# Optimization experiments

Measured on AMD Instinct MI355X. Metric: run time of the kernel, lower is better.

## Reference

```python
import jax, jax.numpy as jnp
import numpy as np

DIM = 256
NUM_ITERS = 5
NUM_CLASSES = 365
TRIU_LEN = DIM * (DIM + 1) // 2  # 32896

# lower-triangular (incl. diag) flat indices in row-major order, matching
# torch.ones(d,d).triu().t().reshape(-1).nonzero()
_TRIL_IDX = np.nonzero(np.tril(np.ones((DIM, DIM), np.bool_)).reshape(-1))[0]


def setup_inputs() -> dict:
    key = jax.random.key(0)
    k1, k2 = jax.random.split(key)
    B = 64
    x = jax.random.normal(k1, (B, DIM, 14, 14), dtype=jnp.float32)
    fc_w = jax.random.normal(k2, (NUM_CLASSES, TRIU_LEN), dtype=jnp.float32) * 0.01
    fc_b = jnp.zeros((NUM_CLASSES,), dtype=jnp.float32)
    return {"x": x, "fc_w": fc_w, "fc_b": fc_b}


def _cov(x):
    # x: [B, D, H, W] -> centered second-order pooling [B, D, D]
    B, D, H, W = x.shape
    M = H * W
    xf = x.reshape(B, D, M)
    xc = xf - jnp.mean(xf, axis=2, keepdims=True)
    # x @ I_hat @ x^T == (xc @ xf^T) / M == (xc @ xc^T) / M
    y = jnp.einsum('bdm,bem->bde', xc, xc) / M
    return y + 1e-7 * jnp.eye(D, dtype=x.dtype)


def _matrix_sqrt_ns(a, num_iters):
    # Newton-Schulz iteration for matrix square root; a: [B, D, D]
    B, D, _ = a.shape
    I = jnp.eye(D, dtype=a.dtype)
    normA = jnp.trace(a, axis1=1, axis2=2)  # [B]
    Y = a / normA[:, None, None]
    Z = jnp.broadcast_to(I, (B, D, D))
    for _ in range(num_iters):
        T = 0.5 * (3.0 * I - jnp.einsum('bij,bjk->bik', Z, Y))
        Y = jnp.einsum('bij,bjk->bik', Y, T)
        Z = jnp.einsum('bij,bjk->bik', T, Z)
    return Y * jnp.sqrt(normA)[:, None, None]


def _triu(x):
    # gather lower-tri (== upper-tri of symmetric cov) entries: [B, D, D] -> [B, D(D+1)/2]
    B, D, _ = x.shape
    return x.reshape(B, D * D)[:, _TRIL_IDX]


def reference(x, fc_w, fc_b):
    y = _cov(x)
    y = _matrix_sqrt_ns(y, NUM_ITERS)
    y = _triu(y)
    return y @ fc_w.T + fc_b
```

## Files before the change

### kernel.cpp

```cpp
#include <hip/hip_runtime.h>
#include <hip/hip_bf16.h>

typedef __attribute__((ext_vector_type(8))) short bf16x8;
typedef __attribute__((ext_vector_type(4))) float f32x4;

static __device__ __forceinline__ ushort f2b(float f) {
    unsigned u = __float_as_uint(f);
    return (ushort)((u + 0x7fffu + ((u >> 16) & 1u)) >> 16);
}

static __device__ __forceinline__ void gload16(const void* g, void* lds) {
    __builtin_amdgcn_global_load_lds(
        (const __attribute__((address_space(1))) unsigned int*)g,
        (__attribute__((address_space(3))) unsigned int*)lds, 16, 0, 0);
}

__global__ __launch_bounds__(256) void prep_kernel(
    const float* __restrict__ x, ushort* __restrict__ xc, float* __restrict__ var)
{
    const int t = threadIdx.x, wv = t >> 6, l = t & 63;
    const int bid = blockIdx.x;
    const int x8 = bid & 7, rr = bid >> 3;
    const int dgrp = rr & 63, bgrp = rr >> 6;
    const int b = bgrp * 8 + x8;
    const int rowid = b * 256 + dgrp * 4 + wv;
    const float* xr = x + (size_t)rowid * 196;

    float x0 = xr[l];
    float x1 = xr[l + 64];
    float x2 = xr[l + 128];
    float x3 = (l < 4) ? xr[l + 192] : 0.0f;

    float s1 = x0 + x1 + x2 + x3;
    float s2 = x0*x0 + x1*x1 + x2*x2 + x3*x3;
    #pragma unroll
    for (int off = 32; off; off >>= 1) {
        s1 += __shfl_xor(s1, off);
        s2 += __shfl_xor(s2, off);
    }
    const float mean = s1 * (1.0f / 196.0f);
    if (l == 0) var[rowid] = s2 * (1.0f / 196.0f) - mean * mean + 1e-7f;

    ushort* xcr = xc + (size_t)rowid * 256;
    xcr[l]       = f2b(x0 - mean);
    xcr[l + 64]  = f2b(x1 - mean);
    xcr[l + 128] = f2b(x2 - mean);
    xcr[l + 192] = (l < 4) ? f2b(x3 - mean) : (ushort)0;
}

template<int MODE>
__global__ __launch_bounds__(256) void gemm_ns(
    const ushort* __restrict__ A, const ushort* __restrict__ A2,
    const ushort* __restrict__ Bt,
    ushort* __restrict__ C, ushort* __restrict__ C2,
    const float* __restrict__ var)
{
    __shared__ ushort As[2][2][128][32];
    __shared__ ushort Bs[2][2][128][32];
    __shared__ float tr_s[4];

    const int bid = blockIdx.x, x8 = bid & 7;
    int b, i0, j0;
    bool useA2 = false;
    if (MODE == 2) {
        const int tt = (bid >> 3) & 3;
        useA2 = ((bid >> 5) & 1) != 0;
        b = (bid >> 6) * 8 + x8;
        i0 = (tt >> 1) * 128; j0 = (tt & 1) * 128;
    } else if (MODE == 3) {
        const int rr = bid >> 3, t3 = rr % 3;
        b = (rr / 3) * 8 + x8;
        i0 = (t3 == 0) ? 0 : 128;
        j0 = (t3 == 2) ? 128 : 0;
    } else {
        const int tt = (bid >> 3) & 3;
        b = (bid >> 5) * 8 + x8;
        i0 = (tt >> 1) * 128; j0 = (tt & 1) * 128;
    }
    const ushort* Ab  = (useA2 ? A2 : A) + (size_t)b * 65536;
    const ushort* Btb = Bt + (size_t)b * 65536;

    const int t = threadIdx.x, wv = t >> 6, l = t & 63;
    const int li = l & 15, hi = l >> 4;
    const int wr = wv >> 1, wc = wv & 1;
    const int lrow = l >> 2;
    const int seg = (l & 3) * 8;

#define STAGE(buf, ck) do {                                                     \
    _Pragma("unroll")                                                           \
    for (int it = 0; it < 4; ++it) {                                            \
        const int c16 = wv * 4 + it;                                 \
        const int tk = c16 >> 3, r16 = c16 & 7;                                 \
        const int row = r16 * 16 + lrow;                                        \
        gload16(Ab + (size_t)(i0 + row) * 256 + (ck) * 64 + tk * 32 + seg,      \
                (char*)&As[buf][0][0][0] + tk * 8192 + r16 * 1024);             \
        gload16(Btb + (size_t)(j0 + row) * 256 + (ck) * 64 + tk * 32 + seg,     \
                (char*)&Bs[buf][0][0][0] + tk * 8192 + r16 * 1024);             \
    }                                                                           \
} while (0)

    STAGE(0, 0);
    if (MODE == 0 || MODE == 3) {
        float v = var[b * 256 + t];
        #pragma unroll
        for (int off = 32; off; off >>= 1) v += __shfl_xor(v, off);
        if (l == 0) tr_s[wv] = v;
    }
    __syncthreads();
    float trace = 0.f;
    if (MODE == 0 || MODE == 3) trace = tr_s[0] + tr_s[1] + tr_s[2] + tr_s[3];

    f32x4 acc[4][4];
    #pragma unroll
    for (int m = 0; m < 4; ++m)
        #pragma unroll
        for (int n = 0; n < 4; ++n) acc[m][n] = (f32x4){0.f, 0.f, 0.f, 0.f};

    int cur = 0;
    #pragma unroll
    for (int ck = 0; ck < 4; ++ck) {
        if (ck < 3) STAGE(cur ^ 1, ck + 1);
        #pragma unroll
        for (int s = 0; s < 2; ++s) {
            bf16x8 af[4], bfr[4];
            #pragma unroll
            for (int m = 0; m < 4; ++m)
                af[m] = *(const bf16x8*)&As[cur][s][wr * 64 + m * 16 + li][hi * 8];
            #pragma unroll
            for (int n = 0; n < 4; ++n)
                bfr[n] = *(const bf16x8*)&Bs[cur][s][wc * 64 + n * 16 + li][hi * 8];
            #pragma unroll
            for (int m = 0; m < 4; ++m)
                #pragma unroll
                for (int n = 0; n < 4; ++n)
                    acc[m][n] = __builtin_amdgcn_mfma_f32_16x16x32_bf16(
                        af[m], bfr[n], acc[m][n], 0, 0, 0);
        }
        __syncthreads();
        cur ^= 1;
    }
#undef STAGE

    if (MODE == 3) {
        const float sc = sqrtf(trace);
        ushort* trib = C + (size_t)b * 32896;
        #pragma unroll
        for (int m = 0; m < 4; ++m)
            #pragma unroll
            for (int n = 0; n < 4; ++n)
                #pragma unroll
                for (int r = 0; r < 4; ++r) {
                    const int gi = i0 + wr * 64 + m * 16 + hi * 4 + r;
                    const int gj = j0 + wc * 64 + n * 16 + li;
                    if (gj <= gi)
                        trib[(gi * (gi + 1)) / 2 + gj] = f2b(acc[m][n][r] * sc);
                }
    } else {
        const float invtr = (MODE == 0) ? (1.0f / trace) : 0.0f;
        ushort* Cb  = ((MODE == 2 && useA2) ? C2 : C) + (size_t)b * 65536;
        ushort* C2b = (MODE == 0) ? (C2 + (size_t)b * 65536) : nullptr;
        #pragma unroll
        for (int m = 0; m < 4; ++m)
            #pragma unroll
            for (int n = 0; n < 4; ++n)
                #pragma unroll
                for (int r = 0; r < 4; ++r) {
                    const int gi = i0 + wr * 64 + m * 16 + hi * 4 + r;
                    const int gj = j0 + wc * 64 + n * 16 + li;
                    const float v = acc[m][n][r];
                    const size_t idx = (size_t)gi * 256 + gj;
                    if (MODE == 0) {
                        float y0 = (v * (1.0f / 196.0f) + ((gi == gj) ? 1e-7f : 0.0f)) * invtr;
                        Cb[idx]  = f2b(y0);
                        C2b[idx] = f2b(((gi == gj) ? 1.5f : 0.0f) - 0.5f * y0);
                    } else if (MODE == 1) {
                        Cb[idx] = f2b(((gi == gj) ? 1.5f : 0.0f) - 0.5f * v);
                    } else {
                        Cb[idx] = f2b(v);
                    }
                }
    }
}

__global__ __launch_bounds__(256) void fc_gemm(
    const ushort* __restrict__ tri, const float* __restrict__ W,
    float* __restrict__ partial)
{
    __shared__ ushort Asl[4][64][32];
    __shared__ float  Wsl[4][64][32];

    const int ntile = blockIdx.x;
    const int split = blockIdx.y;
    const int steps = 12 + (split < 8 ? 1 : 0);
    const int step0 = split * 12 + (split < 8 ? split : 8);

    const int tid = threadIdx.x, wv = tid >> 6, l = tid & 63;
    const int li = l & 15, hi = l >> 4;

    const int arow = tid >> 2, aseg = tid & 3;
    const int wrow0 = tid >> 3, wseg = tid & 7;
    const int wrow1 = 32 + (tid >> 3);
    const int wcl0 = min(ntile * 64 + wrow0, 364);
    const int wcl1 = min(ntile * 64 + wrow1, 364);

#define FSTAGE(s) do {                                                          \
    const int kk_ = (step0 + (s)) * 32;                                         \
    const int r_ = (s) & 3;                                                     \
    gload16(tri + (size_t)arow * 32896 + kk_ + aseg * 8,                        \
            &Asl[r_][arow][aseg * 8]);                                          \
    gload16(W + (size_t)wcl0 * 32896 + kk_ + wseg * 4,                          \
            &Wsl[r_][wrow0][wseg * 4]);                                         \
    gload16(W + (size_t)wcl1 * 32896 + kk_ + wseg * 4,                          \
            &Wsl[r_][wrow1][wseg * 4]);                                         \
} while (0)

    FSTAGE(0); FSTAGE(1); FSTAGE(2);

    f32x4 acc[4];
    #pragma unroll
    for (int m = 0; m < 4; ++m) acc[m] = (f32x4){0.f, 0.f, 0.f, 0.f};

    for (int s = 0; s < steps; ++s) {
        if (s + 3 < steps) FSTAGE(s + 3);
        asm volatile("s_waitcnt vmcnt(9)" ::: "memory");
        __builtin_amdgcn_sched_barrier(0);
        __builtin_amdgcn_s_barrier();

        const int r = s & 3;
        const float4 wf0 = *(const float4*)&Wsl[r][wv * 16 + li][hi * 8];
        const float4 wf1 = *(const float4*)&Wsl[r][wv * 16 + li][hi * 8 + 4];
        bf16x8 bfr;
        bfr[0] = (short)f2b(wf0.x); bfr[1] = (short)f2b(wf0.y);
        bfr[2] = (short)f2b(wf0.z); bfr[3] = (short)f2b(wf0.w);
        bfr[4] = (short)f2b(wf1.x); bfr[5] = (short)f2b(wf1.y);
        bfr[6] = (short)f2b(wf1.z); bfr[7] = (short)f2b(wf1.w);

        bf16x8 af[4];
        #pragma unroll
        for (int m = 0; m < 4; ++m)
            af[m] = *(const bf16x8*)&Asl[r][m * 16 + li][hi * 8];
        #pragma unroll
        for (int m = 0; m < 4; ++m)
            acc[m] = __builtin_amdgcn_mfma_f32_16x16x32_bf16(af[m], bfr, acc[m], 0, 0, 0);

        __builtin_amdgcn_s_barrier();
    }
#undef FSTAGE

    #pragma unroll
    for (int m = 0; m < 4; ++m)
        #pragma unroll
        for (int rr = 0; rr < 4; ++rr) {
            const int i = m * 16 + hi * 4 + rr;
            const int j = ntile * 64 + wv * 16 + li;
            partial[((size_t)split * 64 + i) * 384 + j] = acc[m][rr];
        }
}

__global__ void fc_reduce(const float* __restrict__ partial,
                          const float* __restrict__ bias, float* __restrict__ out)
{
    const int idx = blockIdx.x * 256 + threadIdx.x;
    if (idx >= 64 * 365) return;
    const int b = idx / 365, n = idx % 365;
    float s = bias[n];
    #pragma unroll 5
    for (int sp = 0; sp < 85; ++sp)
        s += partial[((size_t)sp * 64 + b) * 384 + n];
    out[idx] = s;
}

extern "C" void kernel_launch(void* const* d_in, const int* in_sizes, int n_in,
                              void* d_out, int out_size, void* d_ws, size_t ws_size,
                              hipStream_t stream)
{
    (void)in_sizes; (void)n_in; (void)out_size; (void)ws_size;
    const float* x   = (const float*)d_in[0];
    const float* fcw = (const float*)d_in[1];
    const float* fcb = (const float*)d_in[2];
    float* out = (float*)d_out;
    char* ws = (char*)d_ws;

    const size_t MS = (size_t)64 * 256 * 256 * 2;
    ushort* w0 = (ushort*)(ws + 0 * MS);
    ushort* w1 = (ushort*)(ws + 1 * MS);
    ushort* w2 = (ushort*)(ws + 2 * MS);
    ushort* w3 = (ushort*)(ws + 3 * MS);
    ushort* w4 = (ushort*)(ws + 4 * MS);
    ushort* xc = (ushort*)(ws + 5 * MS);
    float*  var    = (float*)(ws + 6 * MS);
    ushort* tri    = (ushort*)(ws + 6 * MS + 131072);
    float*  partial= (float*)(ws + 6 * MS + 131072 + 4210688);

    prep_kernel<<<4096, 256, 0, stream>>>(x, xc, var);

    gemm_ns<0><<<256, 256, 0, stream>>>(xc, nullptr, xc, w0, w1, var);
    gemm_ns<4><<<256, 256, 0, stream>>>(w0, nullptr, w1, w2, nullptr, nullptr);
    gemm_ns<1><<<256, 256, 0, stream>>>(w1, nullptr, w2, w0, nullptr, nullptr);
    gemm_ns<2><<<512, 256, 0, stream>>>(w2, w1, w0, w3, w4, nullptr);
    gemm_ns<1><<<256, 256, 0, stream>>>(w4, nullptr, w3, w0, nullptr, nullptr);
    gemm_ns<2><<<512, 256, 0, stream>>>(w3, w4, w0, w1, w2, nullptr);
    gemm_ns<1><<<256, 256, 0, stream>>>(w2, nullptr, w1, w0, nullptr, nullptr);
    gemm_ns<2><<<512, 256, 0, stream>>>(w1, w2, w0, w3, w4, nullptr);
    gemm_ns<1><<<256, 256, 0, stream>>>(w4, nullptr, w3, w0, nullptr, nullptr);
    gemm_ns<3><<<192, 256, 0, stream>>>(w3, nullptr, w0, tri, nullptr, var);

    fc_gemm<<<dim3(6, 85), 256, 0, stream>>>(tri, fcw, partial);
    fc_reduce<<<(64 * 365 + 255) / 256, 256, 0, stream>>>(partial, fcb, out);
}
```

Baseline: 115.1 us.

## Replace double-buffered K loop with 4-stage LDS ring using explicit vmcnt waits

Restructures the GEMM main loop from two large double-buffered chunks into eight 32-wide K steps over a four-slot LDS ring, prefetching three stages ahead. Each step waits on a partial vmcnt count and a raw s_barrier instead of a full __syncthreads drain, aiming to keep more global loads in flight while the MFMAs run. The trace reduction now relies on the loop barriers for visibility. The hand-set vmcnt counts are fragile if the compiler emits other vector-memory ops, and the extra barriers per step add synchronisation cost.

```diff
diff --git a/kernel.cpp b/kernel.cpp
--- a/kernel.cpp
+++ b/kernel.cpp
@@ -55,8 +55,8 @@
     ushort* __restrict__ C, ushort* __restrict__ C2,
     const float* __restrict__ var)
 {
-    __shared__ ushort As[2][2][128][32];
-    __shared__ ushort Bs[2][2][128][32];
+    __shared__ ushort As[4][128][32];
+    __shared__ ushort Bs[4][128][32];
     __shared__ float tr_s[4];
 
     const int bid = blockIdx.x, x8 = bid & 7;
@@ -83,32 +83,27 @@
     const int t = threadIdx.x, wv = t >> 6, l = t & 63;
     const int li = l & 15, hi = l >> 4;
     const int wr = wv >> 1, wc = wv & 1;
-    const int lrow = l >> 2;
-    const int seg = (l & 3) * 8;
-
-#define STAGE(buf, ck) do {                                                     \
-    _Pragma("unroll")                                                           \
-    for (int it = 0; it < 4; ++it) {                                            \
-        const int c16 = wv * 4 + it;                                 \
-        const int tk = c16 >> 3, r16 = c16 & 7;                                 \
-        const int row = r16 * 16 + lrow;                                        \
-        gload16(Ab + (size_t)(i0 + row) * 256 + (ck) * 64 + tk * 32 + seg,      \
-                (char*)&As[buf][0][0][0] + tk * 8192 + r16 * 1024);             \
-        gload16(Btb + (size_t)(j0 + row) * 256 + (ck) * 64 + tk * 32 + seg,     \
-                (char*)&Bs[buf][0][0][0] + tk * 8192 + r16 * 1024);             \
-    }                                                                           \
-} while (0)
-
-    STAGE(0, 0);
+    const int r0 = t >> 2;
+    const int c0 = (t & 3) * 8;
+
+    float trace = 0.f;
     if (MODE == 0 || MODE == 3) {
         float v = var[b * 256 + t];
         #pragma unroll
         for (int off = 32; off; off >>= 1) v += __shfl_xor(v, off);
         if (l == 0) tr_s[wv] = v;
     }
-    __syncthreads();
-    float trace = 0.f;
-    if (MODE == 0 || MODE == 3) trace = tr_s[0] + tr_s[1] + tr_s[2] + tr_s[3];
+
+#define GSTAGE(s) do {                                                          \
+    const int r_ = (s) & 3;                                                     \
+    const int kk = (s) * 32;                                                    \
+    gload16(Ab  + (size_t)(i0 + r0) * 256 + kk + c0,      &As[r_][r0][c0]);     \
+    gload16(Ab  + (size_t)(i0 + 64 + r0) * 256 + kk + c0, &As[r_][64 + r0][c0]);\
+    gload16(Btb + (size_t)(j0 + r0) * 256 + kk + c0,      &Bs[r_][r0][c0]);     \
+    gload16(Btb + (size_t)(j0 + 64 + r0) * 256 + kk + c0, &Bs[r_][64 + r0][c0]);\
+} while (0)
+
+    GSTAGE(0); GSTAGE(1); GSTAGE(2);
 
     f32x4 acc[4][4];
     #pragma unroll
@@ -116,30 +111,36 @@
         #pragma unroll
         for (int n = 0; n < 4; ++n) acc[m][n] = (f32x4){0.f, 0.f, 0.f, 0.f};
 
-    int cur = 0;
-    #pragma unroll
-    for (int ck = 0; ck < 4; ++ck) {
-        if (ck < 3) STAGE(cur ^ 1, ck + 1);
-        #pragma unroll
-        for (int s = 0; s < 2; ++s) {
-            bf16x8 af[4], bfr[4];
-            #pragma unroll
-            for (int m = 0; m < 4; ++m)
-                af[m] = *(const bf16x8*)&As[cur][s][wr * 64 + m * 16 + li][hi * 8];
+    #pragma unroll
+    for (int s = 0; s < 8; ++s) {
+        if (s < 5) GSTAGE(s + 3);
+        if (s < 5)      asm volatile("s_waitcnt vmcnt(12)" ::: "memory");
+        else if (s == 5) asm volatile("s_waitcnt vmcnt(8)" ::: "memory");
+        else if (s == 6) asm volatile("s_waitcnt vmcnt(4)" ::: "memory");
+        else             asm volatile("s_waitcnt vmcnt(0)" ::: "memory");
+        __builtin_amdgcn_sched_barrier(0);
+        __builtin_amdgcn_s_barrier();
+
+        const int r = s & 3;
+        bf16x8 af[4], bfr[4];
+        #pragma unroll
+        for (int m = 0; m < 4; ++m)
+            af[m] = *(const bf16x8*)&As[r][wr * 64 + m * 16 + li][hi * 8];
+        #pragma unroll
+        for (int n = 0; n < 4; ++n)
+            bfr[n] = *(const bf16x8*)&Bs[r][wc * 64 + n * 16 + li][hi * 8];
+        #pragma unroll
+        for (int m = 0; m < 4; ++m)
             #pragma unroll
             for (int n = 0; n < 4; ++n)
-                bfr[n] = *(const bf16x8*)&Bs[cur][s][wc * 64 + n * 16 + li][hi * 8];
-            #pragma unroll
-            for (int m = 0; m < 4; ++m)
-                #pragma unroll
-                for (int n = 0; n < 4; ++n)
-                    acc[m][n] = __builtin_amdgcn_mfma_f32_16x16x32_bf16(
-                        af[m], bfr[n], acc[m][n], 0, 0, 0);
-        }
-        __syncthreads();
-        cur ^= 1;
-    }
-#undef STAGE
+                acc[m][n] = __builtin_amdgcn_mfma_f32_16x16x32_bf16(
+                    af[m], bfr[n], acc[m][n], 0, 0, 0);
+
+        __builtin_amdgcn_s_barrier();
+    }
+#undef GSTAGE
+
+    if (MODE == 0 || MODE == 3) trace = tr_s[0] + tr_s[1] + tr_s[2] + tr_s[3];
 
     if (MODE == 3) {
         const float sc = sqrtf(trace);
```

Result: no change. 113.6 us (-1.3%).
